# Performance work log

Hardware: AMD Instinct MI355X
Metric: run time of the kernel (lower is better)

The kernel has to match this reference:

```python
import jax, jax.numpy as jnp
import numpy as np

N = 50000
E = 800000
DESC = 256
IN_CH = DESC + 64  # 320
HEADS = 4
HC = 64  # hidden_channels // heads
HID = HEADS * HC  # 256


def _lin(k, fan_in, fan_out):
    kw, kb = jax.random.split(k)
    s = 1.0 / np.sqrt(fan_in)
    W = jax.random.uniform(kw, (fan_in, fan_out), minval=-s, maxval=s, dtype=jnp.float32)
    b = jax.random.uniform(kb, (fan_out,), minval=-s, maxval=s, dtype=jnp.float32)
    return W, b


def setup_inputs() -> dict:
    key = jax.random.key(0)
    ks = jax.random.split(key, 16)
    x = jax.random.normal(ks[0], (N, DESC), dtype=jnp.float32)
    kpts = jax.random.uniform(ks[1], (N, 2), dtype=jnp.float32) * jnp.array([1216.0, 352.0])
    pts_3d = jax.random.uniform(ks[2], (N, 3), dtype=jnp.float32) * 10.0
    edge_index = jax.random.randint(ks[3], (2, E), 0, N, dtype=jnp.int64)

    W1, b1 = _lin(ks[4], 3, 32)
    W2, b2 = _lin(ks[5], 32, 64)
    Wres, bres = _lin(ks[6], IN_CH, HID)
    Wl, bl = _lin(ks[7], IN_CH, HID)
    Wr, br = _lin(ks[8], IN_CH, HID)
    We, _ = _lin(ks[9], 3, HID)
    att = jax.random.normal(ks[10], (HEADS, HC), dtype=jnp.float32) * 0.1
    conv_bias = jnp.zeros((HID,), dtype=jnp.float32)
    gamma = jnp.ones((HID,), dtype=jnp.float32)
    beta = jnp.zeros((HID,), dtype=jnp.float32)
    Wp, bp = _lin(ks[11], HID, 256)
    return dict(x=x, kpts=kpts, pts_3d=pts_3d, edge_index=edge_index,
                W1=W1, b1=b1, W2=W2, b2=b2, Wres=Wres, bres=bres,
                Wl=Wl, bl=bl, Wr=Wr, br=br, We=We, att=att, conv_bias=conv_bias,
                gamma=gamma, beta=beta, Wp=Wp, bp=bp)


def reference(x, kpts, pts_3d, edge_index, W1, b1, W2, b2, Wres, bres,
              Wl, bl, Wr, br, We, att, conv_bias, gamma, beta, Wp, bp):
    n = x.shape[0]
    norm_uv = kpts / jnp.array([1216.0, 352.0], dtype=kpts.dtype)
    depth = pts_3d[:, 2:3]
    pos_input = jnp.concatenate([norm_uv, depth], axis=-1)  # [N,3]
    pos_feat = jax.nn.silu(pos_input @ W1 + b1) @ W2 + b2   # [N,64]
    node_x = jnp.concatenate([x, pos_feat], axis=-1)        # [N,320]

    src, dst = edge_index[0], edge_index[1]
    rel_uv = norm_uv[dst] - norm_uv[src]                    # [E,2]
    dist = jnp.linalg.norm(rel_uv, axis=-1, keepdims=True)  # [E,1]
    edge_attr = jnp.concatenate([rel_uv, dist], axis=-1)    # [E,3]

    identity = node_x @ Wres + bres                         # [N,256]

    # GATv2Conv (share_weights=False, concat=True, neg_slope=0.2, no self-loops)
    x_l = (node_x @ Wl + bl).reshape(n, HEADS, HC)
    x_r = (node_x @ Wr + br).reshape(n, HEADS, HC)
    e_feat = (edge_attr @ We).reshape(-1, HEADS, HC)        # [E,H,C]

    m = x_l[src] + x_r[dst] + e_feat                        # [E,H,C]
    m = jnp.where(m >= 0, m, 0.2 * m)                       # LeakyReLU(0.2)
    logits = jnp.einsum('ehc,hc->eh', m, att)               # [E,H]

    # segment softmax over incoming edges of each dst node
    lmax = jax.ops.segment_max(logits, dst, num_segments=n)  # [N,H]
    ex = jnp.exp(logits - lmax[dst])
    denom = jax.ops.segment_sum(ex, dst, num_segments=n)     # [N,H]
    alpha = ex / (denom[dst] + 1e-16)                        # [E,H]

    msg = x_l[src] * alpha[:, :, None]                       # [E,H,C]
    out = jax.ops.segment_sum(msg, dst, num_segments=n).reshape(n, HID) + conv_bias

    # LayerNorm
    mu = out.mean(-1, keepdims=True)
    var = out.var(-1, keepdims=True)
    out = (out - mu) / jnp.sqrt(var + 1e-5) * gamma + beta

    out = jax.nn.silu(out)
    out = out + identity
    out = out @ Wp + bp
    return out, alpha
```

## Files before the change

### kernel.cpp

```cpp
#include <hip/hip_runtime.h>
#include <math.h>

#define NN 50000
#define NPAD 50048
#define EE 800000
#define HIDC 256
#define INCH 320

typedef __attribute__((ext_vector_type(8))) short bf16x8;
typedef __attribute__((ext_vector_type(4))) float f32x4;
typedef __attribute__((ext_vector_type(2))) float f32x2;

static __device__ __forceinline__ float4 ld4(const float* p){ return *(const float4*)p; }

static __device__ __forceinline__ unsigned short f2b(float f){
  union { float f; unsigned u; } v; v.f = f;
  unsigned r = v.u + 0x7fffu + ((v.u >> 16) & 1u);
  return (unsigned short)(r >> 16);
}
static __device__ __forceinline__ float b2f(unsigned short u){
  union { unsigned u; float f; } v; v.u = ((unsigned)u) << 16; return v.f;
}
static __device__ __forceinline__ float rlane_f(float v, int l){
  return __uint_as_float(__builtin_amdgcn_readlane(__float_as_uint(v), l));
}
static __device__ __forceinline__ int rlane_i(int v, int l){
  return __builtin_amdgcn_readlane(v, l);
}
static __device__ __forceinline__ f32x2 unpk(unsigned u){
  f32x2 r;
  r.x = __uint_as_float(u << 16);
  r.y = __uint_as_float(u & 0xffff0000u);
  return r;
}
static __device__ __forceinline__ f32x2 fma2(f32x2 a, f32x2 b, f32x2 c){
  return __builtin_elementwise_fma(a, b, c);
}
static __device__ __forceinline__ f32x2 max2(f32x2 a, f32x2 b){
  return __builtin_elementwise_max(a, b);
}
static __device__ __forceinline__ f32x2 set2(float v){ f32x2 r; r.x = v; r.y = v; return r; }

typedef const __attribute__((address_space(1))) unsigned int* gas_u32;
typedef __attribute__((address_space(3))) unsigned int* las_u32;
static __device__ __forceinline__ void gload_lds16(const void* g, void* l){
  __builtin_amdgcn_global_load_lds((gas_u32)g, (las_u32)l, 16, 0, 0);
}

__global__ void cvt_x_kernel(const float* __restrict__ x, unsigned short* __restrict__ nodex)
{
  int t = blockIdx.x*blockDim.x + threadIdx.x;
  int row = t >> 6;
  if (row >= NN) return;
  int c4 = (t & 63) * 4;
  float4 v = ld4(x + (size_t)row*256 + c4);
  ushort4 o;
  o.x = f2b(v.x); o.y = f2b(v.y); o.z = f2b(v.z); o.w = f2b(v.w);
  *(ushort4*)(nodex + (size_t)row*320 + c4) = o;
}

__global__ void node_mlp_kernel(const float* __restrict__ kpts,
                                const float* __restrict__ pts3d,
                                const float* __restrict__ W1, const float* __restrict__ b1,
                                const float* __restrict__ W2, const float* __restrict__ b2,
                                unsigned short* __restrict__ nodex)
{
  int i = blockIdx.x*blockDim.x + threadIdx.x;
  if (i >= NN) return;
  float u = kpts[2*i]   * (1.0f/1216.0f);
  float v = kpts[2*i+1] * (1.0f/352.0f);
  float d = pts3d[3*i+2];
  float h[32];
#pragma unroll
  for (int j=0;j<32;++j){
    float t = u*W1[j] + v*W1[32+j] + d*W1[64+j] + b1[j];
    h[j] = t / (1.0f + __expf(-t));
  }
  for (int o=0;o<64;o+=4){
    float s0=b2[o], s1=b2[o+1], s2=b2[o+2], s3=b2[o+3];
#pragma unroll
    for (int j=0;j<32;++j){
      float hj = h[j];
      const float* w = W2 + j*64 + o;
      s0 += hj*w[0]; s1 += hj*w[1]; s2 += hj*w[2]; s3 += hj*w[3];
    }
    ushort4 r; r.x=f2b(s0); r.y=f2b(s1); r.z=f2b(s2); r.w=f2b(s3);
    *(ushort4*)(nodex + (size_t)i*320 + 256 + o) = r;
  }
}

__global__ void cvt_w_kernel(const float* __restrict__ Wres, const float* __restrict__ Wl,
                             const float* __restrict__ Wr,   const float* __restrict__ Wp,
                             const float* __restrict__ bres, const float* __restrict__ bl,
                             const float* __restrict__ br,
                             unsigned short* __restrict__ wt, float* __restrict__ biascat)
{
  int t = blockIdx.x*blockDim.x + threadIdx.x;
  if (t < 245760) {
    int which = t / 81920;
    int rem = t % 81920;
    int n = rem / 320, k = rem % 320;
    const float* W = (which == 0) ? Wres : (which == 1) ? Wl : Wr;
    wt[(size_t)which*81920 + rem] = f2b(W[(size_t)k*256 + n]);
  } else if (t < 311296) {
    int r = t - 245760;
    int n = r / 256, k = r % 256;
    wt[245760 + r] = f2b(Wp[(size_t)k*256 + n]);
  } else {
    int r = t - 311296;
    const float* src = (r < 256) ? bres : (r < 512) ? bl : br;
    biascat[r] = src[r & 255];
  }
}

#define GK 32
__global__ __launch_bounds__(256) void mfma_gemm_kernel(
    const unsigned short* __restrict__ A,
    const unsigned short* __restrict__ BT,
    const float* __restrict__ bias,
    float* __restrict__ Cf,
    unsigned short* __restrict__ Cx1,
    unsigned short* __restrict__ Cx2,
    int M, int K)
{
  __shared__ unsigned short Als[128*GK];
  __shared__ unsigned short Bls[128*GK];
  int tid = threadIdx.x;
  int lane = tid & 63, wave = tid >> 6;
  int wm = (wave >> 1) * 64, wn = (wave & 1) * 64;
  int row0 = blockIdx.x * 128, col0 = blockIdx.y * 128;

  f32x4 acc[4][4];
#pragma unroll
  for (int i=0;i<4;++i)
#pragma unroll
    for (int j=0;j<4;++j){ acc[i][j].x=0.f; acc[i][j].y=0.f; acc[i][j].z=0.f; acc[i][j].w=0.f; }

  int fm = lane & 15;
  int fk = (lane >> 4) * 8;

  for (int k0 = 0; k0 < K; k0 += GK) {
#pragma unroll
    for (int it = 0; it < 2; ++it) {
      int seg = it*256 + tid;
      int r = seg >> 2, kb = (seg & 3) * 8;
      gload_lds16(A  + (size_t)(row0 + r)*K + k0 + kb, Als + (it*256 + wave*64)*8);
      gload_lds16(BT + (size_t)(col0 + r)*K + k0 + kb, Bls + (it*256 + wave*64)*8);
    }
    __syncthreads();

    bf16x8 af[4], bfr[4];
#pragma unroll
    for (int mi=0; mi<4; ++mi)
      af[mi] = *(const bf16x8*)&Als[(wm + mi*16 + fm)*GK + fk];
#pragma unroll
    for (int ni=0; ni<4; ++ni)
      bfr[ni] = *(const bf16x8*)&Bls[(wn + ni*16 + fm)*GK + fk];
#pragma unroll
    for (int mi=0; mi<4; ++mi)
#pragma unroll
      for (int ni=0; ni<4; ++ni)
        acc[mi][ni] = __builtin_amdgcn_mfma_f32_16x16x32_bf16(af[mi], bfr[ni], acc[mi][ni], 0, 0, 0);
    __syncthreads();
  }

  int seg = col0 >> 8;
  int colbase = col0 - seg*256;
  int cn = lane & 15, cr = (lane >> 4) * 4;
#pragma unroll
  for (int ni=0; ni<4; ++ni){
    int gcol = col0 + wn + ni*16 + cn;
    int col  = colbase + wn + ni*16 + cn;
    float bb = bias[gcol];
#pragma unroll
    for (int mi=0; mi<4; ++mi){
#pragma unroll
      for (int r=0; r<4; ++r){
        int row = row0 + wm + mi*16 + cr + r;
        if (row < M){
          float v = acc[mi][ni][r] + bb;
          if (seg == 0)      Cf [(size_t)row*256 + col] = v;
          else if (seg == 1) Cx1[(size_t)row*256 + col] = f2b(v);
          else               Cx2[(size_t)row*256 + col] = f2b(v);
        }
      }
    }
  }
}

__global__ void hist_kernel(const int* __restrict__ ei, int* __restrict__ deg){
  int e = blockIdx.x*blockDim.x + threadIdx.x;
  if (e < EE) atomicAdd(&deg[ei[EE + e]], 1);
}

__global__ __launch_bounds__(1024) void scan1_kernel(const int* __restrict__ deg,
                                                     int* __restrict__ incl, int* __restrict__ bsum){
  __shared__ int wsums[16];
  int t = threadIdx.x, lane = t & 63, w = t >> 6;
  int i = blockIdx.x*1024 + t;
  int v = (i < NN) ? deg[i] : 0;
  int sc = v;
#pragma unroll
  for (int off = 1; off < 64; off <<= 1) {
    int o = __shfl_up(sc, off, 64);
    if (lane >= off) sc += o;
  }
  if (lane == 63) wsums[w] = sc;
  __syncthreads();
  if (w == 0) {
    int ws = (lane < 16) ? wsums[lane] : 0;
#pragma unroll
    for (int off = 1; off < 16; off <<= 1) {
      int o = __shfl_up(ws, off, 64);
      if (lane >= off) ws += o;
    }
    if (lane < 16) wsums[lane] = ws;
  }
  __syncthreads();
  int woff = (w > 0) ? wsums[w-1] : 0;
  if (i < NN) incl[i] = sc + woff;
  if (t == 1023) bsum[blockIdx.x] = woff + sc;
}

__global__ void scan2_kernel(int* __restrict__ bsum, int nblk){
  int lane = threadIdx.x;
  int v = (lane < nblk) ? bsum[lane] : 0;
#pragma unroll
  for (int off = 1; off < 64; off <<= 1) {
    int o = __shfl_up(v, off, 64);
    if (lane >= off) v += o;
  }
  if (lane < nblk) bsum[lane] = v;
}

__global__ __launch_bounds__(1024) void scan3_kernel(const int* __restrict__ incl,
                                                     const int* __restrict__ deg,
                                                     const int* __restrict__ bsum,
                                                     int* __restrict__ rowptr, int* __restrict__ cursor,
                                                     int nblk){
  int i = blockIdx.x*1024 + threadIdx.x;
  if (i < NN) {
    int b = blockIdx.x;
    int prev = (b > 0) ? bsum[b-1] : 0;
    int ex = prev + incl[i] - deg[i];
    rowptr[i] = ex;
    cursor[i] = ex;
  }
  if (i == 0) rowptr[NN] = bsum[nblk-1];
}

__global__ void scatter_kernel(const int* __restrict__ ei, const float* __restrict__ kpts,
                               int* __restrict__ cursor,
                               float4* __restrict__ edata, int* __restrict__ eord){
  int e = blockIdx.x*blockDim.x + threadIdx.x;
  if (e >= EE) return;
  int s = ei[e];
  int d = ei[EE + e];
  int pos = atomicAdd(&cursor[d], 1);
  float su = kpts[2*s]   * (1.0f/1216.0f);
  float sv = kpts[2*s+1] * (1.0f/352.0f);
  float du = kpts[2*d]   * (1.0f/1216.0f);
  float dv = kpts[2*d+1] * (1.0f/352.0f);
  float ru = du - su, rv = dv - sv;
  float dist = sqrtf(ru*ru + rv*rv);
  float4 ed; ed.x = ru; ed.y = rv; ed.z = dist; ed.w = __int_as_float(s);
  edata[pos] = ed;
  eord[pos] = e;
}

#define LOAD8(Q, B0)                                               \
  if ((B0) < cnt) {                                                \
    _Pragma("unroll")                                              \
    for (int t = 0; t < 8; ++t) {                                  \
      int sj = rlane_i(s, ((B0) + t) & 63);                        \
      Q[t] = *(const uint2*)(xlp + ((size_t)sj << 8));             \
    }                                                              \
  }

#define PROC8(Q, B0)                                               \
  _Pragma("unroll")                                                \
  for (int t = 0; t < 8; ++t) {                                    \
    int j = (B0) + t;                                              \
    if (j < cnt) {                                                 \
      float ruj = rlane_f(ed.x, j);                                \
      float rvj = rlane_f(ed.y, j);                                \
      float dj  = rlane_f(ed.z, j);                                \
      f32x2 x01 = unpk(Q[t].x), x23 = unpk(Q[t].y);                \
      f32x2 t01 = fma2(set2(ruj), we0a, xr01);                     \
      t01 = fma2(set2(rvj), we1a, t01);                            \
      t01 = fma2(set2(dj),  we2a, t01);                            \
      t01 = t01 + x01;                                             \
      f32x2 t23 = fma2(set2(ruj), we0b, xr23);                     \
      t23 = fma2(set2(rvj), we1b, t23);                            \
      t23 = fma2(set2(dj),  we2b, t23);                            \
      t23 = t23 + x23;                                             \
      t01 = max2(t01, t01*0.2f);                                   \
      t23 = max2(t23, t23*0.2f);                                   \
      f32x2 pd = t01*atta;                                         \
      pd = fma2(t23, attb, pd);                                    \
      float p = pd.x + pd.y;                                       \
      p += __shfl_xor(p, 1, 64);                                   \
      p += __shfl_xor(p, 2, 64);                                   \
      p += __shfl_xor(p, 4, 64);                                   \
      p += __shfl_xor(p, 8, 64);                                   \
      float exv = __expf(p);                                       \
      denom += exv;                                                \
      int ej = rlane_i(e, j);                                      \
      if ((lane & 15) == 0) alpha_out[(size_t)ej*4 + head] = exv;  \
      f32x2 ex2 = set2(exv);                                       \
      agg01 = fma2(ex2, x01, agg01);                               \
      agg23 = fma2(ex2, x23, agg23);                               \
    }                                                              \
  }

__global__ __launch_bounds__(256) void node_attn_kernel(
    const float4* __restrict__ edata, const int* __restrict__ eord,
    const unsigned short* __restrict__ xl, const unsigned short* __restrict__ xr,
    const float* __restrict__ We, const float* __restrict__ att,
    const float* __restrict__ cbias, const float* __restrict__ gamma,
    const float* __restrict__ beta,
    const int* __restrict__ rowptr,
    const float* __restrict__ identity,
    float* __restrict__ alpha_out, float* __restrict__ denom_buf,
    unsigned short* __restrict__ hbuf)
{
  int wid  = threadIdx.x >> 6;
  int lane = threadIdx.x & 63;
  int v = blockIdx.x*4 + wid;
  if (v >= NN) return;
  int c0 = lane*4;
  int head = lane >> 4;

  f32x2 we0a, we0b, we1a, we1b, we2a, we2b, atta, attb;
  we0a.x = We[c0];       we0a.y = We[c0+1];       we0b.x = We[c0+2];       we0b.y = We[c0+3];
  we1a.x = We[256+c0];   we1a.y = We[256+c0+1];   we1b.x = We[256+c0+2];   we1b.y = We[256+c0+3];
  we2a.x = We[512+c0];   we2a.y = We[512+c0+1];   we2b.x = We[512+c0+2];   we2b.y = We[512+c0+3];
  atta.x = att[c0];      atta.y = att[c0+1];      attb.x = att[c0+2];      attb.y = att[c0+3];
  uint2 xrq = *(const uint2*)(xr + (size_t)v*256 + c0);
  f32x2 xr01 = unpk(xrq.x), xr23 = unpk(xrq.y);
  const unsigned short* xlp = xl + c0;

  int rs = rowptr[v], re = rowptr[v+1];
  int deg = re - rs;

  float denom = 0.f;
  f32x2 agg01 = set2(0.f), agg23 = set2(0.f);

  for (int base = 0; base < deg; base += 64) {
    int cnt = min(64, deg - base);
    float4 ed; ed.x = 0.f; ed.y = 0.f; ed.z = 0.f; ed.w = __int_as_float(0);
    int e = 0;
    if (lane < cnt) {
      ed = edata[rs + base + lane];
      e  = eord [rs + base + lane];
    }
    int s = __float_as_int(ed.w);

    uint2 qa[8], qb[8];
    LOAD8(qa, 0);
    for (int b0 = 0; b0 < cnt; b0 += 16) {
      LOAD8(qb, b0 + 8);
      PROC8(qa, b0);
      LOAD8(qa, b0 + 16);
      PROC8(qb, b0 + 8);
    }
  }

  float rdenom = 1.0f / (denom + 1e-16f);
  if ((lane & 15) == 0) denom_buf[(size_t)v*4 + head] = denom;

  float a0 = agg01.x*rdenom + cbias[c0];
  float a1 = agg01.y*rdenom + cbias[c0+1];
  float a2 = agg23.x*rdenom + cbias[c0+2];
  float a3 = agg23.y*rdenom + cbias[c0+3];

  float ps  = a0 + a1 + a2 + a3;
  float ps2 = a0*a0 + a1*a1 + a2*a2 + a3*a3;
#pragma unroll
  for (int off = 1; off < 64; off <<= 1) {
    ps  += __shfl_xor(ps,  off, 64);
    ps2 += __shfl_xor(ps2, off, 64);
  }
  float mu  = ps  * (1.0f/256.0f);
  float var = ps2 * (1.0f/256.0f) - mu*mu;
  float rstd = rsqrtf(var + 1e-5f);
  float4 g  = ld4(gamma + c0);
  float4 b  = ld4(beta  + c0);
  float4 idv = ld4(identity + (size_t)v*256 + c0);
  float y0 = (a0 - mu)*rstd*g.x + b.x;
  float y1 = (a1 - mu)*rstd*g.y + b.y;
  float y2 = (a2 - mu)*rstd*g.z + b.z;
  float y3 = (a3 - mu)*rstd*g.w + b.w;
  y0 = y0 / (1.0f + __expf(-y0)) + idv.x;
  y1 = y1 / (1.0f + __expf(-y1)) + idv.y;
  y2 = y2 / (1.0f + __expf(-y2)) + idv.z;
  y3 = y3 / (1.0f + __expf(-y3)) + idv.w;
  ushort4 hq; hq.x=f2b(y0); hq.y=f2b(y1); hq.z=f2b(y2); hq.w=f2b(y3);
  *(ushort4*)(hbuf + (size_t)v*256 + c0) = hq;
}

__global__ void alpha_fin_kernel(const int* __restrict__ ei, const float* __restrict__ denom_buf,
                                 float* __restrict__ alpha)
{
  int e = blockIdx.x*blockDim.x + threadIdx.x;
  if (e >= EE) return;
  int d = ei[EE + e];
  float4 dn = ld4(denom_buf + (size_t)d*4);
  float4 a = ld4(alpha + (size_t)e*4);
  a.x /= (dn.x + 1e-16f);
  a.y /= (dn.y + 1e-16f);
  a.z /= (dn.z + 1e-16f);
  a.w /= (dn.w + 1e-16f);
  *(float4*)(alpha + (size_t)e*4) = a;
}

extern "C" void kernel_launch(void* const* d_in, const int* in_sizes, int n_in,
                              void* d_out, int out_size, void* d_ws, size_t ws_size,
                              hipStream_t stream)
{
  const float* x      = (const float*)d_in[0];
  const float* kpts   = (const float*)d_in[1];
  const float* pts3d  = (const float*)d_in[2];
  const int*   ei     = (const int*)d_in[3];
  const float* W1     = (const float*)d_in[4];
  const float* b1     = (const float*)d_in[5];
  const float* W2     = (const float*)d_in[6];
  const float* b2     = (const float*)d_in[7];
  const float* Wres   = (const float*)d_in[8];
  const float* bres   = (const float*)d_in[9];
  const float* Wl     = (const float*)d_in[10];
  const float* bl     = (const float*)d_in[11];
  const float* Wr     = (const float*)d_in[12];
  const float* br     = (const float*)d_in[13];
  const float* We     = (const float*)d_in[14];
  const float* att    = (const float*)d_in[15];
  const float* cbias  = (const float*)d_in[16];
  const float* gamma  = (const float*)d_in[17];
  const float* beta   = (const float*)d_in[18];
  const float* Wp     = (const float*)d_in[19];
  const float* bp     = (const float*)d_in[20];

  float* out       = (float*)d_out;
  float* alpha_out = out + (size_t)NN*HIDC;

  float* wsf = (float*)d_ws;
  float*          identity = wsf;
  unsigned short* xl       = (unsigned short*)(wsf + 12800000);
  unsigned short* xr       = (unsigned short*)(wsf + 19206144);
  unsigned short* nodex    = (unsigned short*)(wsf + 25612288);
  unsigned short* hbuf     = (unsigned short*)(wsf + 25612288);
  unsigned short* wt       = (unsigned short*)(wsf + 33619968);
  float*          biascat  = wsf + 33775616;
  float*          denomb   = wsf + 33776384;
  float4*         edata    = (float4*)(wsf + 33976384);
  int*            eord     = (int*)(wsf + 37176384);
  int*            incl     = (int*)(wsf + 37176384);
  int*            deg      = (int*)(wsf + 37976384);
  int*            rowptr   = (int*)(wsf + 38026384);
  int*            cursor   = (int*)(wsf + 38076385);
  int*            bsum     = (int*)(wsf + 38126385);

  unsigned short* wtcat = wt;
  unsigned short* wtp   = wt + 245760;

  cvt_x_kernel<<<12500, 256, 0, stream>>>(x, nodex);
  node_mlp_kernel<<<(NN+255)/256, 256, 0, stream>>>(kpts, pts3d, W1, b1, W2, b2, nodex);
  cvt_w_kernel<<<1219, 256, 0, stream>>>(Wres, Wl, Wr, Wp, bres, bl, br, wt, biascat);

  dim3 g3(NPAD/128, 6);
  mfma_gemm_kernel<<<g3, 256, 0, stream>>>(nodex, wtcat, biascat, identity, xl, xr, NN, INCH);

  hipMemsetAsync(deg, 0, NN*sizeof(int), stream);
  hist_kernel<<<(EE+255)/256, 256, 0, stream>>>(ei, deg);
  int nblk = (NN + 1023) / 1024;
  scan1_kernel<<<nblk, 1024, 0, stream>>>(deg, incl, bsum);
  scan2_kernel<<<1, 64, 0, stream>>>(bsum, nblk);
  scan3_kernel<<<nblk, 1024, 0, stream>>>(incl, deg, bsum, rowptr, cursor, nblk);
  scatter_kernel<<<(EE+255)/256, 256, 0, stream>>>(ei, kpts, cursor, edata, eord);

  node_attn_kernel<<<(NN+3)/4, 256, 0, stream>>>(edata, eord, xl, xr, We, att,
                                                 cbias, gamma, beta,
                                                 rowptr, identity,
                                                 alpha_out, denomb, hbuf);
  alpha_fin_kernel<<<(EE+255)/256, 256, 0, stream>>>(ei, denomb, alpha_out);

  dim3 g1(NPAD/128, 2);
  mfma_gemm_kernel<<<g1, 256, 0, stream>>>(hbuf, wtp, bp, out, nullptr, nullptr, NN, HIDC);
}
```

Baseline: 557.9 us.

## Process four edges per wavefront iteration with 16 lanes per edge

Restructures the per-node attention loop so each 16-lane group handles one edge, with each lane owning 16 channels. Four edges are processed in parallel per iteration with a one-step prefetch of the next 32-byte x_l rows, and partial aggregates are reduced across groups at the end. This is meant to cut the per-edge serial chain of readlanes and shuffle reductions and to widen the gathers, at the cost of more registers and a cross-group reduction of 16 values plus the denominator.

```diff
diff --git a/kernel.cpp b/kernel.cpp
--- a/kernel.cpp
+++ b/kernel.cpp
@@ -20,12 +20,6 @@
 }
 static __device__ __forceinline__ float b2f(unsigned short u){
   union { unsigned u; float f; } v; v.u = ((unsigned)u) << 16; return v.f;
-}
-static __device__ __forceinline__ float rlane_f(float v, int l){
-  return __uint_as_float(__builtin_amdgcn_readlane(__float_as_uint(v), l));
-}
-static __device__ __forceinline__ int rlane_i(int v, int l){
-  return __builtin_amdgcn_readlane(v, l);
 }
 static __device__ __forceinline__ f32x2 unpk(unsigned u){
   f32x2 r;
@@ -268,51 +262,6 @@
   eord[pos] = e;
 }
 
-#define LOAD8(Q, B0)                                               \
-  if ((B0) < cnt) {                                                \
-    _Pragma("unroll")                                              \
-    for (int t = 0; t < 8; ++t) {                                  \
-      int sj = rlane_i(s, ((B0) + t) & 63);                        \
-      Q[t] = *(const uint2*)(xlp + ((size_t)sj << 8));             \
-    }                                                              \
-  }
-
-#define PROC8(Q, B0)                                               \
-  _Pragma("unroll")                                                \
-  for (int t = 0; t < 8; ++t) {                                    \
-    int j = (B0) + t;                                              \
-    if (j < cnt) {                                                 \
-      float ruj = rlane_f(ed.x, j);                                \
-      float rvj = rlane_f(ed.y, j);                                \
-      float dj  = rlane_f(ed.z, j);                                \
-      f32x2 x01 = unpk(Q[t].x), x23 = unpk(Q[t].y);                \
-      f32x2 t01 = fma2(set2(ruj), we0a, xr01);                     \
-      t01 = fma2(set2(rvj), we1a, t01);                            \
-      t01 = fma2(set2(dj),  we2a, t01);                            \
-      t01 = t01 + x01;                                             \
-      f32x2 t23 = fma2(set2(ruj), we0b, xr23);                     \
-      t23 = fma2(set2(rvj), we1b, t23);                            \
-      t23 = fma2(set2(dj),  we2b, t23);                            \
-      t23 = t23 + x23;                                             \
-      t01 = max2(t01, t01*0.2f);                                   \
-      t23 = max2(t23, t23*0.2f);                                   \
-      f32x2 pd = t01*atta;                                         \
-      pd = fma2(t23, attb, pd);                                    \
-      float p = pd.x + pd.y;                                       \
-      p += __shfl_xor(p, 1, 64);                                   \
-      p += __shfl_xor(p, 2, 64);                                   \
-      p += __shfl_xor(p, 4, 64);                                   \
-      p += __shfl_xor(p, 8, 64);                                   \
-      float exv = __expf(p);                                       \
-      denom += exv;                                                \
-      int ej = rlane_i(e, j);                                      \
-      if ((lane & 15) == 0) alpha_out[(size_t)ej*4 + head] = exv;  \
-      f32x2 ex2 = set2(exv);                                       \
-      agg01 = fma2(ex2, x01, agg01);                               \
-      agg23 = fma2(ex2, x23, agg23);                               \
-    }                                                              \
-  }
-
 __global__ __launch_bounds__(256) void node_attn_kernel(
     const float4* __restrict__ edata, const int* __restrict__ eord,
     const unsigned short* __restrict__ xl, const unsigned short* __restrict__ xr,
@@ -328,27 +277,39 @@
   int lane = threadIdx.x & 63;
   int v = blockIdx.x*4 + wid;
   if (v >= NN) return;
-  int c0 = lane*4;
-  int head = lane >> 4;
-
-  f32x2 we0a, we0b, we1a, we1b, we2a, we2b, atta, attb;
-  we0a.x = We[c0];       we0a.y = We[c0+1];       we0b.x = We[c0+2];       we0b.y = We[c0+3];
-  we1a.x = We[256+c0];   we1a.y = We[256+c0+1];   we1b.x = We[256+c0+2];   we1b.y = We[256+c0+3];
-  we2a.x = We[512+c0];   we2a.y = We[512+c0+1];   we2b.x = We[512+c0+2];   we2b.y = We[512+c0+3];
-  atta.x = att[c0];      atta.y = att[c0+1];      attb.x = att[c0+2];      attb.y = att[c0+3];
-  uint2 xrq = *(const uint2*)(xr + (size_t)v*256 + c0);
-  f32x2 xr01 = unpk(xrq.x), xr23 = unpk(xrq.y);
-  const unsigned short* xlp = xl + c0;
+  int sub = lane & 15;
+  int g   = lane >> 4;
+  int c0  = sub * 16;
+  int head = sub >> 2;
+
+  f32x2 w0[8], w1[8], w2[8], at[8], xrv[8];
+#pragma unroll
+  for (int i=0;i<8;++i){
+    w0[i] = *(const f32x2*)(We + c0 + 2*i);
+    w1[i] = *(const f32x2*)(We + 256 + c0 + 2*i);
+    w2[i] = *(const f32x2*)(We + 512 + c0 + 2*i);
+    at[i] = *(const f32x2*)(att + c0 + 2*i);
+  }
+  {
+    uint4 xq0 = *(const uint4*)(xr + (size_t)v*256 + c0);
+    uint4 xq1 = *(const uint4*)(xr + (size_t)v*256 + c0 + 8);
+    xrv[0]=unpk(xq0.x); xrv[1]=unpk(xq0.y); xrv[2]=unpk(xq0.z); xrv[3]=unpk(xq0.w);
+    xrv[4]=unpk(xq1.x); xrv[5]=unpk(xq1.y); xrv[6]=unpk(xq1.z); xrv[7]=unpk(xq1.w);
+  }
 
   int rs = rowptr[v], re = rowptr[v+1];
   int deg = re - rs;
 
   float denom = 0.f;
-  f32x2 agg01 = set2(0.f), agg23 = set2(0.f);
+  f32x2 agg[8];
+#pragma unroll
+  for (int i=0;i<8;++i) agg[i] = set2(0.f);
+
+  const unsigned short* xlp = xl + c0;
 
   for (int base = 0; base < deg; base += 64) {
     int cnt = min(64, deg - base);
-    float4 ed; ed.x = 0.f; ed.y = 0.f; ed.z = 0.f; ed.w = __int_as_float(0);
+    float4 ed; ed.x=0.f; ed.y=0.f; ed.z=0.f; ed.w=__int_as_float(0);
     int e = 0;
     if (lane < cnt) {
       ed = edata[rs + base + lane];
@@ -356,47 +317,101 @@
     }
     int s = __float_as_int(ed.w);
 
-    uint2 qa[8], qb[8];
-    LOAD8(qa, 0);
-    for (int b0 = 0; b0 < cnt; b0 += 16) {
-      LOAD8(qb, b0 + 8);
-      PROC8(qa, b0);
-      LOAD8(qa, b0 + 16);
-      PROC8(qb, b0 + 8);
-    }
-  }
-
+    uint4 qa0, qa1, qb0, qb1;
+    {
+      int sj = __shfl(s, g, 64);
+      const unsigned short* p = xlp + ((size_t)sj << 8);
+      qa0 = *(const uint4*)p; qa1 = *(const uint4*)(p + 8);
+    }
+    for (int j4 = 0; j4 < cnt; j4 += 4) {
+      if (j4 + 4 < cnt) {
+        int sj = __shfl(s, j4 + 4 + g, 64);
+        const unsigned short* p = xlp + ((size_t)sj << 8);
+        qb0 = *(const uint4*)p; qb1 = *(const uint4*)(p + 8);
+      }
+      int jj = j4 + g;
+      float ruj = __shfl(ed.x, jj, 64);
+      float rvj = __shfl(ed.y, jj, 64);
+      float dj  = __shfl(ed.z, jj, 64);
+      int   ej  = __shfl(e,    jj, 64);
+      bool valid = jj < cnt;
+
+      f32x2 xv[8];
+      xv[0]=unpk(qa0.x); xv[1]=unpk(qa0.y); xv[2]=unpk(qa0.z); xv[3]=unpk(qa0.w);
+      xv[4]=unpk(qa1.x); xv[5]=unpk(qa1.y); xv[6]=unpk(qa1.z); xv[7]=unpk(qa1.w);
+
+      f32x2 vru = set2(ruj), vrv = set2(rvj), vd = set2(dj);
+      f32x2 dot = set2(0.f);
+#pragma unroll
+      for (int i=0;i<8;++i){
+        f32x2 t = fma2(vru, w0[i], xrv[i]);
+        t = fma2(vrv, w1[i], t);
+        t = fma2(vd,  w2[i], t);
+        t = t + xv[i];
+        t = max2(t, t*0.2f);
+        dot = fma2(t, at[i], dot);
+      }
+      float p = dot.x + dot.y;
+      p += __shfl_xor(p, 1, 64);
+      p += __shfl_xor(p, 2, 64);
+      float exv = valid ? __expf(p) : 0.f;
+      denom += exv;
+      if (valid && (sub & 3) == 0) alpha_out[(size_t)ej*4 + head] = exv;
+      f32x2 ex2 = set2(exv);
+#pragma unroll
+      for (int i=0;i<8;++i) agg[i] = fma2(ex2, xv[i], agg[i]);
+      qa0 = qb0; qa1 = qb1;
+    }
+  }
+
+#pragma unroll
+  for (int off = 16; off < 64; off <<= 1) {
+    denom += __shfl_xor(denom, off, 64);
+#pragma unroll
+    for (int i=0;i<8;++i){
+      agg[i].x += __shfl_xor(agg[i].x, off, 64);
+      agg[i].y += __shfl_xor(agg[i].y, off, 64);
+    }
+  }
+  if (g == 0 && (sub & 3) == 0) denom_buf[(size_t)v*4 + head] = denom;
   float rdenom = 1.0f / (denom + 1e-16f);
-  if ((lane & 15) == 0) denom_buf[(size_t)v*4 + head] = denom;
-
-  float a0 = agg01.x*rdenom + cbias[c0];
-  float a1 = agg01.y*rdenom + cbias[c0+1];
-  float a2 = agg23.x*rdenom + cbias[c0+2];
-  float a3 = agg23.y*rdenom + cbias[c0+3];
-
-  float ps  = a0 + a1 + a2 + a3;
-  float ps2 = a0*a0 + a1*a1 + a2*a2 + a3*a3;
-#pragma unroll
-  for (int off = 1; off < 64; off <<= 1) {
+
+  float a[16];
+#pragma unroll
+  for (int i=0;i<8;++i){
+    f32x2 cb = *(const f32x2*)(cbias + c0 + 2*i);
+    a[2*i]   = agg[i].x * rdenom + cb.x;
+    a[2*i+1] = agg[i].y * rdenom + cb.y;
+  }
+  float ps = 0.f, ps2 = 0.f;
+#pragma unroll
+  for (int i=0;i<16;++i){ ps += a[i]; ps2 += a[i]*a[i]; }
+#pragma unroll
+  for (int off = 1; off < 16; off <<= 1) {
     ps  += __shfl_xor(ps,  off, 64);
     ps2 += __shfl_xor(ps2, off, 64);
   }
   float mu  = ps  * (1.0f/256.0f);
   float var = ps2 * (1.0f/256.0f) - mu*mu;
   float rstd = rsqrtf(var + 1e-5f);
-  float4 g  = ld4(gamma + c0);
-  float4 b  = ld4(beta  + c0);
-  float4 idv = ld4(identity + (size_t)v*256 + c0);
-  float y0 = (a0 - mu)*rstd*g.x + b.x;
-  float y1 = (a1 - mu)*rstd*g.y + b.y;
-  float y2 = (a2 - mu)*rstd*g.z + b.z;
-  float y3 = (a3 - mu)*rstd*g.w + b.w;
-  y0 = y0 / (1.0f + __expf(-y0)) + idv.x;
-  y1 = y1 / (1.0f + __expf(-y1)) + idv.y;
-  y2 = y2 / (1.0f + __expf(-y2)) + idv.z;
-  y3 = y3 / (1.0f + __expf(-y3)) + idv.w;
-  ushort4 hq; hq.x=f2b(y0); hq.y=f2b(y1); hq.z=f2b(y2); hq.w=f2b(y3);
-  *(ushort4*)(hbuf + (size_t)v*256 + c0) = hq;
+  if (g == 0) {
+    unsigned outp[8];
+#pragma unroll
+    for (int i=0;i<8;++i){
+      f32x2 gm = *(const f32x2*)(gamma + c0 + 2*i);
+      f32x2 bt = *(const f32x2*)(beta  + c0 + 2*i);
+      f32x2 iv = *(const f32x2*)(identity + (size_t)v*256 + c0 + 2*i);
+      float y0 = (a[2*i]   - mu)*rstd*gm.x + bt.x;
+      float y1 = (a[2*i+1] - mu)*rstd*gm.y + bt.y;
+      y0 = y0 / (1.0f + __expf(-y0)) + iv.x;
+      y1 = y1 / (1.0f + __expf(-y1)) + iv.y;
+      outp[i] = (unsigned)f2b(y0) | ((unsigned)f2b(y1) << 16);
+    }
+    uint4 o0; o0.x=outp[0]; o0.y=outp[1]; o0.z=outp[2]; o0.w=outp[3];
+    uint4 o1; o1.x=outp[4]; o1.y=outp[5]; o1.z=outp[6]; o1.w=outp[7];
+    *(uint4*)(hbuf + (size_t)v*256 + c0) = o0;
+    *(uint4*)(hbuf + (size_t)v*256 + c0 + 8) = o1;
+  }
 }
 
 __global__ void alpha_fin_kernel(const int* __restrict__ ei, const float* __restrict__ denom_buf,
```

Result: slower. 596.8 us (+7.0%).
